# Kernel optimization log

Hardware: AMD Instinct MI355X
Metric: run time of the kernel (lower is better)

The kernel has to match this reference:

```python
import jax, jax.numpy as jnp
import numpy as np

B, L, D, H, VOCAB = 8, 1024, 1024, 8, 32000
DH = D // H  # dim_per_head = 128
SCALE = float((DH // H) ** (-0.5))  # faithful to key.size(-1)//num_heads
EPS = 1e-5


def setup_inputs() -> dict:
    key = jax.random.key(0)
    ks = jax.random.split(key, 12)
    tokens = jax.random.randint(ks[0], (B, L), 0, VOCAB)
    s = 0.02
    emb = jax.random.normal(ks[1], (VOCAB, D), jnp.float32) * s
    emb = emb.at[0].set(0.0)  # padding_idx=0
    Wq = jax.random.normal(ks[2], (D, D), jnp.float32) * s
    Wk = jax.random.normal(ks[3], (D, D), jnp.float32) * s
    Wv = jax.random.normal(ks[4], (D, D), jnp.float32) * s
    Wo = jax.random.normal(ks[5], (D, D), jnp.float32) * s
    bq = jnp.zeros((D,), jnp.float32)
    bk = jnp.zeros((D,), jnp.float32)
    bv = jnp.zeros((D,), jnp.float32)
    bo = jnp.zeros((D,), jnp.float32)
    gamma = jnp.ones((2 * D,), jnp.float32)
    beta = jnp.zeros((2 * D,), jnp.float32)
    return {"tokens": tokens, "emb": emb, "Wq": Wq, "bq": bq, "Wk": Wk,
            "bk": bk, "Wv": Wv, "bv": bv, "Wo": Wo, "bo": bo,
            "gamma": gamma, "beta": beta}


def reference(tokens, emb, Wq, bq, Wk, bk, Wv, bv, Wo, bo, gamma, beta):
    # padding mask: [B, L, L] True where key token == 0
    pad = (tokens == 0)  # [B, L]
    mask = jnp.broadcast_to(pad[:, None, :], (B, L, L))
    mask = jnp.tile(mask, (H, 1, 1))  # torch .repeat(num_heads,1,1) -> [H*B, L, L]

    x = emb[tokens]  # [B, L, D]

    q = (x @ Wq + bq).reshape(B * H, L, DH)  # faithful interleaved view
    k = (x @ Wk + bk).reshape(B * H, L, DH)
    v = (x @ Wv + bv).reshape(B * H, L, DH)

    scores = jnp.einsum('bqd,bkd->bqk', q, k) * SCALE
    scores = jnp.where(mask, -jnp.inf, scores)
    attn = jax.nn.softmax(scores, axis=-1)
    ctx = jnp.einsum('bqk,bkd->bqd', attn, v).reshape(B, L, D)

    out = ctx @ Wo + bo  # [B, L, D]
    r = x + out
    maxpool = r.max(axis=1)   # [B, D]
    meanpool = r.mean(axis=1)  # [B, D]
    agg = jnp.concatenate([maxpool, meanpool], axis=1)  # [B, 2D]

    mu = agg.mean(axis=-1, keepdims=True)
    var = agg.var(axis=-1, keepdims=True)
    return (agg - mu) / jnp.sqrt(var + EPS) * gamma + beta
```

## Files before the change

### kernel.cpp

```cpp
#include <hip/hip_runtime.h>
#include <math.h>

typedef __attribute__((ext_vector_type(8))) short short8;
typedef __attribute__((ext_vector_type(4))) float f32x4;

constexpr int CB = 8, CL = 1024, CD = 1024, CDH = 128, CM = 8192;
constexpr float CSCALE = 0.25f;
constexpr float CEPS = 1e-5f;

__device__ inline ushort f2b(float f) {
    union { float f; unsigned u; } v; v.f = f;
    unsigned r = v.u + 0x7FFF + ((v.u >> 16) & 1);
    return (ushort)(r >> 16);
}
__device__ inline float b2f(ushort u) {
    union { unsigned u; float f; } v; v.u = ((unsigned)u) << 16;
    return v.f;
}

__device__ inline void gld16(const void* g, void* l) {
    __builtin_amdgcn_global_load_lds(
        (const __attribute__((address_space(1))) void*)g,
        (__attribute__((address_space(3))) void*)l, 16, 0, 0);
}

__global__ __launch_bounds__(256) void k_gather(const int* __restrict__ tokens,
                                                const float* __restrict__ emb,
                                                float* __restrict__ x,
                                                ushort* __restrict__ xb) {
    int row = blockIdx.x;
    int tok = tokens[row];
    float4 v = ((const float4*)(emb + (size_t)tok * CD))[threadIdx.x];
    ((float4*)(x + (size_t)row * CD))[threadIdx.x] = v;
    ushort4 o; o.x = f2b(v.x); o.y = f2b(v.y); o.z = f2b(v.z); o.w = f2b(v.w);
    ((ushort4*)(xb + (size_t)row * CD))[threadIdx.x] = o;
}

__global__ __launch_bounds__(256) void k_wtrans(const float* __restrict__ W,
                                                ushort* __restrict__ Wt) {
    __shared__ float ws_[32][33];
    const int tk = blockIdx.x * 32, tn = blockIdx.y * 32;
    const int t = threadIdx.x;
    {
        int r = t >> 3, c4 = (t & 7) * 4;
        *(float4*)&ws_[r][c4] = *(const float4*)&W[(size_t)(tk + r) * CD + tn + c4];
    }
    __syncthreads();
    int n = t >> 3, k4 = (t & 7) * 4;
    ushort4 o;
    o.x = f2b(ws_[k4 + 0][n]); o.y = f2b(ws_[k4 + 1][n]);
    o.z = f2b(ws_[k4 + 2][n]); o.w = f2b(ws_[k4 + 3][n]);
    *(ushort4*)&Wt[(size_t)(tn + n) * CD + tk + k4] = o;
}

__global__ __launch_bounds__(256) void k_gemm_qkv(const ushort* __restrict__ A,
                                                  const ushort* __restrict__ Wt3,
                                                  const float* __restrict__ b0,
                                                  const float* __restrict__ b1,
                                                  const float* __restrict__ b2,
                                                  ushort* __restrict__ C3) {
    __shared__ ushort As[128 * 32];
    __shared__ ushort Bs[128 * 32];
    const int z = blockIdx.z;
    const ushort* Bt  = Wt3 + (size_t)z * CD * CD;
    const float* bias = (z == 0) ? b0 : ((z == 1) ? b1 : b2);
    ushort* Cout      = C3 + (size_t)z * CM * CD;

    const int t = threadIdx.x, w = t >> 6, l = t & 63;
    const int lane15 = l & 15, quad = l >> 4;
    const int bm = blockIdx.y * 128, bn = blockIdx.x * 128;
    const int wm = (w >> 1) * 64, wn = (w & 1) * 64;
    const int arow = l >> 2;
    const int aseg = (l & 3) * 8;
    f32x4 acc[4][4] = {};

    for (int k0 = 0; k0 < CD; k0 += 32) {
        __syncthreads();
        #pragma unroll
        for (int c2 = 0; c2 < 2; ++c2) {
            int c = w * 2 + c2;
            gld16(A  + (size_t)(bm + c * 16 + arow) * CD + k0 + aseg, &As[c * 512 + l * 8]);
            gld16(Bt + (size_t)(bn + c * 16 + arow) * CD + k0 + aseg, &Bs[c * 512 + l * 8]);
        }
        __syncthreads();
        short8 af[4], bf[4];
        #pragma unroll
        for (int im = 0; im < 4; ++im)
            af[im] = *(const short8*)&As[(wm + im * 16 + lane15) * 32 + quad * 8];
        #pragma unroll
        for (int in = 0; in < 4; ++in)
            bf[in] = *(const short8*)&Bs[(wn + in * 16 + lane15) * 32 + quad * 8];
        #pragma unroll
        for (int im = 0; im < 4; ++im)
            #pragma unroll
            for (int in = 0; in < 4; ++in)
                acc[im][in] = __builtin_amdgcn_mfma_f32_16x16x32_bf16(af[im], bf[in], acc[im][in], 0, 0, 0);
    }
    #pragma unroll
    for (int in = 0; in < 4; ++in) {
        int col = bn + wn + in * 16 + lane15;
        float bv = bias[col];
        #pragma unroll
        for (int im = 0; im < 4; ++im) {
            int row0 = bm + wm + im * 16 + quad * 4;
            #pragma unroll
            for (int r = 0; r < 4; ++r)
                Cout[(size_t)(row0 + r) * CD + col] = f2b(acc[im][in][r] + bv);
        }
    }
}

__global__ __launch_bounds__(256) void k_gemm_out(const ushort* __restrict__ A,
                                                  const ushort* __restrict__ Bt,
                                                  const float* __restrict__ bias,
                                                  const float* __restrict__ resid,
                                                  float* __restrict__ pmax,
                                                  float* __restrict__ psum) {
    __shared__ ushort As[128 * 32];
    __shared__ ushort Bs[128 * 32];
    __shared__ float redmx[4][64], redsm[4][64];
    const int t = threadIdx.x, w = t >> 6, l = t & 63;
    const int lane15 = l & 15, quad = l >> 4;
    const int bm = blockIdx.y * 128, bn = blockIdx.x * 128;
    const int wm = (w >> 1) * 64, wn = (w & 1) * 64;
    const int arow = l >> 2;
    const int aseg = (l & 3) * 8;
    f32x4 acc[4][4] = {};

    for (int k0 = 0; k0 < CD; k0 += 32) {
        __syncthreads();
        #pragma unroll
        for (int c2 = 0; c2 < 2; ++c2) {
            int c = w * 2 + c2;
            gld16(A  + (size_t)(bm + c * 16 + arow) * CD + k0 + aseg, &As[c * 512 + l * 8]);
            gld16(Bt + (size_t)(bn + c * 16 + arow) * CD + k0 + aseg, &Bs[c * 512 + l * 8]);
        }
        __syncthreads();
        short8 af[4], bf[4];
        #pragma unroll
        for (int im = 0; im < 4; ++im)
            af[im] = *(const short8*)&As[(wm + im * 16 + lane15) * 32 + quad * 8];
        #pragma unroll
        for (int in = 0; in < 4; ++in)
            bf[in] = *(const short8*)&Bs[(wn + in * 16 + lane15) * 32 + quad * 8];
        #pragma unroll
        for (int im = 0; im < 4; ++im)
            #pragma unroll
            for (int in = 0; in < 4; ++in)
                acc[im][in] = __builtin_amdgcn_mfma_f32_16x16x32_bf16(af[im], bf[in], acc[im][in], 0, 0, 0);
    }
    const int by = blockIdx.y, bb = by >> 3, chunk = by & 7;
    float vmax_[4], vsum_[4];
    #pragma unroll
    for (int in = 0; in < 4; ++in) {
        int col = bn + wn + in * 16 + lane15;
        float bvv = bias[col];
        float mx = -3.4e38f, sm = 0.f;
        #pragma unroll
        for (int im = 0; im < 4; ++im) {
            int row0 = bm + wm + im * 16 + quad * 4;
            #pragma unroll
            for (int r = 0; r < 4; ++r) {
                float rel = acc[im][in][r] + bvv + resid[(size_t)(row0 + r) * CD + col];
                mx = fmaxf(mx, rel);
                sm += rel;
            }
        }
        mx = fmaxf(mx, __shfl_xor(mx, 16));
        mx = fmaxf(mx, __shfl_xor(mx, 32));
        sm += __shfl_xor(sm, 16);
        sm += __shfl_xor(sm, 32);
        vmax_[in] = mx; vsum_[in] = sm;
    }
    if (l < 16) {
        #pragma unroll
        for (int in = 0; in < 4; ++in) {
            redmx[w][in * 16 + lane15] = vmax_[in];
            redsm[w][in * 16 + lane15] = vsum_[in];
        }
    }
    __syncthreads();
    if (t < 128) {
        int wcol = t >> 6, cc = t & 63;
        float m = fmaxf(redmx[wcol][cc], redmx[wcol + 2][cc]);
        float s = redsm[wcol][cc] + redsm[wcol + 2][cc];
        size_t off2 = ((size_t)bb * 8 + chunk) * CD + bn + wcol * 64 + cc;
        pmax[off2] = m;
        psum[off2] = s;
    }
}

__global__ __launch_bounds__(256) void k_vtransp(const ushort* __restrict__ v,
                                                 ushort* __restrict__ Vtp) {
    __shared__ ushort Vs[64 * 136];
    const int i = blockIdx.x >> 4, kt = blockIdx.x & 15;
    const ushort* src = v + (size_t)i * 131072 + (size_t)kt * 64 * 128;
    const int t = threadIdx.x;
    #pragma unroll
    for (int ii = 0; ii < 4; ++ii) {
        int idx = t + 256 * ii;
        int key = idx >> 4, seg = idx & 15;
        *(uint4*)&Vs[key * 136 + seg * 8] = *(const uint4*)&src[key * 128 + seg * 8];
    }
    __syncthreads();
    ushort* dst = Vtp + (size_t)blockIdx.x * 8192;
    #pragma unroll
    for (int it = 0; it < 4; ++it) {
        int L = t + 256 * it;
        int cell = L & 63;
        int quadk = cell >> 4, l15 = cell & 15;
        int p = L >> 6;
        int d = (p >> 1) * 16 + l15;
        int kb = ((p & 1) * 4 + quadk) * 8;
        uint pk[4];
        #pragma unroll
        for (int jj = 0; jj < 4; ++jj) {
            uint lo = Vs[(kb + 2 * jj) * 136 + d];
            uint hi = Vs[(kb + 2 * jj + 1) * 136 + d];
            pk[jj] = lo | (hi << 16);
        }
        *(uint4*)&dst[(size_t)L * 8] = *(uint4*)pk;
    }
}

__global__ __launch_bounds__(512) void k_attn(const ushort* __restrict__ Q,
                                              const ushort* __restrict__ K,
                                              const ushort* __restrict__ Vtp,
                                              const int* __restrict__ tokens,
                                              ushort* __restrict__ ctx) {
    __shared__ ushort Ks[16 * 512];
    __shared__ ushort Vs[16 * 512];
    __shared__ ushort Ps[8 * 1088];
    __shared__ ushort Msk[CL];
    const int i = blockIdx.x, qb = blockIdx.y * 128;
    const int t = threadIdx.x, w = t >> 6, l = t & 63;
    const int lane15 = l & 15, quad = l >> 4;

    {
        const int* tokb = tokens + (i & 7) * CL;
        #pragma unroll
        for (int jj = 0; jj < 2; ++jj) {
            int idx = t + 512 * jj;
            Msk[idx] = (tokb[idx] == 0) ? (ushort)0xFF80 : (ushort)0;
        }
    }
    const int qrow = qb + w * 16 + lane15;
    short8 af[4];
    #pragma unroll
    for (int kc = 0; kc < 4; ++kc)
        af[kc] = *(const short8*)&Q[(size_t)i * 131072 + (size_t)qrow * 128 + kc * 32 + quad * 8];

    f32x4 oacc[8];
    #pragma unroll
    for (int dt = 0; dt < 8; ++dt) oacc[dt] = f32x4{0.f, 0.f, 0.f, 0.f};
    float lsum[4] = {0.f, 0.f, 0.f, 0.f};
    const int wbase = w * 1088;

    for (int kt = 0; kt < 16; ++kt) {
        __syncthreads();
        #pragma unroll
        for (int c = 0; c < 2; ++c) {
            int p = w * 2 + c;
            gld16(K + (size_t)i * 131072 + (size_t)(kt * 64 + (p >> 2) * 16 + lane15) * 128
                    + (p & 3) * 32 + quad * 8,
                  &Ks[p * 512 + l * 8]);
            gld16(Vtp + ((size_t)(i * 16 + kt) * 16 + p) * 512 + l * 8,
                  &Vs[p * 512 + l * 8]);
        }
        __syncthreads();

        f32x4 sc[4];
        #pragma unroll
        for (int j = 0; j < 4; ++j) {
            sc[j] = f32x4{0.f, 0.f, 0.f, 0.f};
            #pragma unroll
            for (int kc = 0; kc < 4; ++kc) {
                short8 bk = *(const short8*)&Ks[(j * 4 + kc) * 512 + l * 8];
                sc[j] = __builtin_amdgcn_mfma_f32_16x16x32_bf16(af[kc], bk, sc[j], 0, 0, 0);
            }
        }
        #pragma unroll
        for (int j = 0; j < 4; ++j) {
            float mj = b2f(Msk[kt * 64 + j * 16 + lane15]);
            #pragma unroll
            for (int r = 0; r < 4; ++r) {
                float p = __expf(fmaf(sc[j][r], CSCALE, mj));
                sc[j][r] = p;
                lsum[r] += p;
            }
        }
        #pragma unroll
        for (int j = 0; j < 4; ++j) {
            int ks2 = j >> 1;
            int qq  = (j & 1) * 2 + (lane15 >> 3);
            int pos = lane15 & 7;
            #pragma unroll
            for (int r = 0; r < 4; ++r) {
                union { float f; unsigned u; } cv; cv.f = sc[j][r];
                Ps[wbase + ks2 * 544 + qq * 136 + (quad * 4 + r) * 8 + pos] =
                    (ushort)(cv.u >> 16);
            }
        }
        short8 ap[2];
        #pragma unroll
        for (int ks2 = 0; ks2 < 2; ++ks2)
            ap[ks2] = *(const short8*)&Ps[wbase + ks2 * 544 + quad * 136 + lane15 * 8];
        #pragma unroll
        for (int dt = 0; dt < 8; ++dt)
            #pragma unroll
            for (int ks2 = 0; ks2 < 2; ++ks2) {
                short8 bv = *(const short8*)&Vs[(dt * 2 + ks2) * 512 + l * 8];
                oacc[dt] = __builtin_amdgcn_mfma_f32_16x16x32_bf16(ap[ks2], bv, oacc[dt], 0, 0, 0);
            }
    }
    float inv[4];
    #pragma unroll
    for (int r = 0; r < 4; ++r) {
        float s = lsum[r];
        #pragma unroll
        for (int off = 1; off < 16; off <<= 1) s += __shfl_xor(s, off);
        inv[r] = 1.f / s;
    }
    #pragma unroll
    for (int dt = 0; dt < 8; ++dt)
        #pragma unroll
        for (int r = 0; r < 4; ++r) {
            int q = qb + w * 16 + quad * 4 + r;
            ctx[(size_t)i * 131072 + (size_t)q * 128 + dt * 16 + lane15] =
                f2b(oacc[dt][r] * inv[r]);
        }
}

__global__ __launch_bounds__(1024) void k_pool2(const float* __restrict__ pmax,
                                                const float* __restrict__ psum,
                                                const float* __restrict__ gamma,
                                                const float* __restrict__ beta,
                                                float* __restrict__ out) {
    __shared__ float rs[16], rq[16];
    __shared__ float s_mu, s_inv;
    const int b = blockIdx.x;
    const int d = threadIdx.x;
    float mx = -3.4e38f, sm = 0.f;
    #pragma unroll
    for (int c = 0; c < 8; ++c) {
        size_t off = ((size_t)b * 8 + c) * CD + d;
        mx = fmaxf(mx, pmax[off]);
        sm += psum[off];
    }
    const float a0 = mx;
    const float a1 = sm * (1.0f / 1024.0f);
    float s = a0 + a1;
    float qd = a0 * a0 + a1 * a1;
    #pragma unroll
    for (int off = 32; off > 0; off >>= 1) {
        s  += __shfl_xor(s, off);
        qd += __shfl_xor(qd, off);
    }
    const int wid = d >> 6;
    if ((d & 63) == 0) { rs[wid] = s; rq[wid] = qd; }
    __syncthreads();
    if (d == 0) {
        float S = 0.f, Qm = 0.f;
        for (int ww = 0; ww < 16; ++ww) { S += rs[ww]; Qm += rq[ww]; }
        float mu  = S * (1.0f / 2048.0f);
        float var = Qm * (1.0f / 2048.0f) - mu * mu;
        s_mu = mu; s_inv = 1.0f / sqrtf(var + CEPS);
    }
    __syncthreads();
    const float mu = s_mu, inv = s_inv;
    out[(size_t)b * 2048 + d]        = (a0 - mu) * inv * gamma[d]        + beta[d];
    out[(size_t)b * 2048 + 1024 + d] = (a1 - mu) * inv * gamma[1024 + d] + beta[1024 + d];
}

extern "C" void kernel_launch(void* const* d_in, const int* in_sizes, int n_in,
                              void* d_out, int out_size, void* d_ws, size_t ws_size,
                              hipStream_t stream) {
    const int*   tokens = (const int*)d_in[0];
    const float* emb    = (const float*)d_in[1];
    const float* Wq     = (const float*)d_in[2];
    const float* bq     = (const float*)d_in[3];
    const float* Wk     = (const float*)d_in[4];
    const float* bk     = (const float*)d_in[5];
    const float* Wv     = (const float*)d_in[6];
    const float* bv     = (const float*)d_in[7];
    const float* Wo     = (const float*)d_in[8];
    const float* bo     = (const float*)d_in[9];
    const float* gamma  = (const float*)d_in[10];
    const float* beta   = (const float*)d_in[11];
    float* out = (float*)d_out;

    char* p = (char*)d_ws;
    float*  x   = (float*)p;   p += (size_t)CM * CD * 4;
    ushort* xb  = (ushort*)p;  p += (size_t)CM * CD * 2;
    ushort* wqt = (ushort*)p;  p += (size_t)CD * CD * 2;
    ushort* wkt = (ushort*)p;  p += (size_t)CD * CD * 2;
    ushort* wvt = (ushort*)p;  p += (size_t)CD * CD * 2;
    ushort* wot = (ushort*)p;  p += (size_t)CD * CD * 2;
    ushort* qb_ = (ushort*)p;  p += (size_t)CM * CD * 2;
    ushort* kb_ = (ushort*)p;  p += (size_t)CM * CD * 2;
    ushort* vb_ = (ushort*)p;  p += (size_t)CM * CD * 2;
    ushort* Vtp = (ushort*)p;  p += (size_t)CM * CD * 2;
    float*  pmax = (float*)p;  p += (size_t)CB * 8 * CD * 4;
    float*  psum = (float*)p;  p += (size_t)CB * 8 * CD * 4;
    ushort* ctx = vb_;

    k_gather<<<CM, 256, 0, stream>>>(tokens, emb, x, xb);

    dim3 wg(32, 32);
    k_wtrans<<<wg, 256, 0, stream>>>(Wq, wqt);
    k_wtrans<<<wg, 256, 0, stream>>>(Wk, wkt);
    k_wtrans<<<wg, 256, 0, stream>>>(Wv, wvt);
    k_wtrans<<<wg, 256, 0, stream>>>(Wo, wot);

    dim3 gq(CD / 128, CM / 128, 3);
    k_gemm_qkv<<<gq, 256, 0, stream>>>(xb, wqt, bq, bk, bv, qb_);

    k_vtransp<<<64 * 16, 256, 0, stream>>>(vb_, Vtp);

    dim3 ag(64, 8);
    k_attn<<<ag, 512, 0, stream>>>(qb_, kb_, Vtp, tokens, ctx);

    dim3 go(CD / 128, CM / 128);
    k_gemm_out<<<go, 256, 0, stream>>>(ctx, wot, bo, x, pmax, psum);

    k_pool2<<<CB, 1024, 0, stream>>>(pmax, psum, gamma, beta, out);
}
```

Measured before the change: 366.2 us.

## Double-buffer K/V tiles in attention and give each wave two query groups

The attention kernel now uses 256 threads per block, and each wave handles 32 query rows as two 16-row groups. Each loaded K and V fragment therefore feeds two MFMAs. K/V tiles are double-buffered in LDS, with the next tile's global-to-LDS load issued before computing on the current one, and only one barrier per iteration. This is meant to hide global load latency and halve LDS fragment reads per MFMA. The cost is more registers (two accumulator sets), double the K/V LDS footprint, and fewer waves per block, which may lower occupancy.

```diff
diff --git a/kernel.cpp b/kernel.cpp
--- a/kernel.cpp
+++ b/kernel.cpp
@@ -223,14 +223,30 @@
     }
 }
 
-__global__ __launch_bounds__(512) void k_attn(const ushort* __restrict__ Q,
+__device__ inline void attn_stage(const ushort* __restrict__ K,
+                                  const ushort* __restrict__ Vtp,
+                                  ushort* KsBuf, ushort* VsBuf,
+                                  int i, int kt, int w, int l,
+                                  int lane15, int quad) {
+    #pragma unroll
+    for (int c = 0; c < 4; ++c) {
+        int p = w * 4 + c;
+        gld16(K + (size_t)i * 131072 + (size_t)(kt * 64 + (p >> 2) * 16 + lane15) * 128
+                + (p & 3) * 32 + quad * 8,
+              KsBuf + p * 512 + (size_t)l * 8);
+        gld16(Vtp + ((size_t)(i * 16 + kt) * 16 + p) * 512 + (size_t)l * 8,
+              VsBuf + p * 512 + (size_t)l * 8);
+    }
+}
+
+__global__ __launch_bounds__(256) void k_attn(const ushort* __restrict__ Q,
                                               const ushort* __restrict__ K,
                                               const ushort* __restrict__ Vtp,
                                               const int* __restrict__ tokens,
                                               ushort* __restrict__ ctx) {
-    __shared__ ushort Ks[16 * 512];
-    __shared__ ushort Vs[16 * 512];
-    __shared__ ushort Ps[8 * 1088];
+    __shared__ ushort Ks[2][16 * 512];
+    __shared__ ushort Vs[2][16 * 512];
+    __shared__ ushort Ps[4 * 1088];
     __shared__ ushort Msk[CL];
     const int i = blockIdx.x, qb = blockIdx.y * 128;
     const int t = threadIdx.x, w = t >> 6, l = t & 63;
@@ -239,96 +255,111 @@
     {
         const int* tokb = tokens + (i & 7) * CL;
         #pragma unroll
-        for (int jj = 0; jj < 2; ++jj) {
-            int idx = t + 512 * jj;
+        for (int jj = 0; jj < 4; ++jj) {
+            int idx = t + 256 * jj;
             Msk[idx] = (tokb[idx] == 0) ? (ushort)0xFF80 : (ushort)0;
         }
     }
-    const int qrow = qb + w * 16 + lane15;
-    short8 af[4];
-    #pragma unroll
-    for (int kc = 0; kc < 4; ++kc)
-        af[kc] = *(const short8*)&Q[(size_t)i * 131072 + (size_t)qrow * 128 + kc * 32 + quad * 8];
-
-    f32x4 oacc[8];
-    #pragma unroll
-    for (int dt = 0; dt < 8; ++dt) oacc[dt] = f32x4{0.f, 0.f, 0.f, 0.f};
-    float lsum[4] = {0.f, 0.f, 0.f, 0.f};
+    short8 af[2][4];
+    #pragma unroll
+    for (int g = 0; g < 2; ++g)
+        #pragma unroll
+        for (int kc = 0; kc < 4; ++kc)
+            af[g][kc] = *(const short8*)&Q[(size_t)i * 131072
+                + (size_t)(qb + w * 32 + g * 16 + lane15) * 128 + kc * 32 + quad * 8];
+
+    f32x4 oacc[2][8];
+    #pragma unroll
+    for (int g = 0; g < 2; ++g)
+        #pragma unroll
+        for (int dt = 0; dt < 8; ++dt) oacc[g][dt] = f32x4{0.f, 0.f, 0.f, 0.f};
+    float lsum[2][4] = {};
     const int wbase = w * 1088;
 
+    attn_stage(K, Vtp, Ks[0], Vs[0], i, 0, w, l, lane15, quad);
+    __syncthreads();
+
     for (int kt = 0; kt < 16; ++kt) {
-        __syncthreads();
-        #pragma unroll
-        for (int c = 0; c < 2; ++c) {
-            int p = w * 2 + c;
-            gld16(K + (size_t)i * 131072 + (size_t)(kt * 64 + (p >> 2) * 16 + lane15) * 128
-                    + (p & 3) * 32 + quad * 8,
-                  &Ks[p * 512 + l * 8]);
-            gld16(Vtp + ((size_t)(i * 16 + kt) * 16 + p) * 512 + l * 8,
-                  &Vs[p * 512 + l * 8]);
-        }
-        __syncthreads();
-
-        f32x4 sc[4];
+        const int cur = kt & 1;
+        if (kt < 15)
+            attn_stage(K, Vtp, Ks[cur ^ 1], Vs[cur ^ 1], i, kt + 1, w, l, lane15, quad);
+
+        f32x4 sc[2][4];
         #pragma unroll
         for (int j = 0; j < 4; ++j) {
-            sc[j] = f32x4{0.f, 0.f, 0.f, 0.f};
-            #pragma unroll
-            for (int kc = 0; kc < 4; ++kc) {
-                short8 bk = *(const short8*)&Ks[(j * 4 + kc) * 512 + l * 8];
-                sc[j] = __builtin_amdgcn_mfma_f32_16x16x32_bf16(af[kc], bk, sc[j], 0, 0, 0);
+            short8 bk[4];
+            #pragma unroll
+            for (int kc = 0; kc < 4; ++kc)
+                bk[kc] = *(const short8*)&Ks[cur][(j * 4 + kc) * 512 + l * 8];
+            #pragma unroll
+            for (int g = 0; g < 2; ++g) {
+                sc[g][j] = f32x4{0.f, 0.f, 0.f, 0.f};
+                #pragma unroll
+                for (int kc = 0; kc < 4; ++kc)
+                    sc[g][j] = __builtin_amdgcn_mfma_f32_16x16x32_bf16(af[g][kc], bk[kc], sc[g][j], 0, 0, 0);
             }
         }
         #pragma unroll
         for (int j = 0; j < 4; ++j) {
             float mj = b2f(Msk[kt * 64 + j * 16 + lane15]);
             #pragma unroll
+            for (int g = 0; g < 2; ++g)
+                #pragma unroll
+                for (int r = 0; r < 4; ++r) {
+                    float pv = __expf(fmaf(sc[g][j][r], CSCALE, mj));
+                    sc[g][j][r] = pv;
+                    lsum[g][r] += pv;
+                }
+        }
+        short8 ap[2][2];
+        #pragma unroll
+        for (int g = 0; g < 2; ++g) {
+            #pragma unroll
+            for (int j = 0; j < 4; ++j) {
+                int ks2 = j >> 1;
+                int qq  = (j & 1) * 2 + (lane15 >> 3);
+                int pos = lane15 & 7;
+                #pragma unroll
+                for (int r = 0; r < 4; ++r) {
+                    union { float f; unsigned u; } cv; cv.f = sc[g][j][r];
+                    Ps[wbase + ks2 * 544 + qq * 136 + (quad * 4 + r) * 8 + pos] =
+                        (ushort)(cv.u >> 16);
+                }
+            }
+            #pragma unroll
+            for (int ks2 = 0; ks2 < 2; ++ks2)
+                ap[g][ks2] = *(const short8*)&Ps[wbase + ks2 * 544 + quad * 136 + lane15 * 8];
+        }
+        #pragma unroll
+        for (int dt = 0; dt < 8; ++dt)
+            #pragma unroll
+            for (int ks2 = 0; ks2 < 2; ++ks2) {
+                short8 bv = *(const short8*)&Vs[cur][(dt * 2 + ks2) * 512 + l * 8];
+                #pragma unroll
+                for (int g = 0; g < 2; ++g)
+                    oacc[g][dt] = __builtin_amdgcn_mfma_f32_16x16x32_bf16(ap[g][ks2], bv, oacc[g][dt], 0, 0, 0);
+            }
+        __syncthreads();
+    }
+    #pragma unroll
+    for (int g = 0; g < 2; ++g) {
+        float inv[4];
+        #pragma unroll
+        for (int r = 0; r < 4; ++r) {
+            float s = lsum[g][r];
+            #pragma unroll
+            for (int off = 1; off < 16; off <<= 1) s += __shfl_xor(s, off);
+            inv[r] = 1.f / s;
+        }
+        #pragma unroll
+        for (int dt = 0; dt < 8; ++dt)
+            #pragma unroll
             for (int r = 0; r < 4; ++r) {
-                float p = __expf(fmaf(sc[j][r], CSCALE, mj));
-                sc[j][r] = p;
-                lsum[r] += p;
+                int q = qb + w * 32 + g * 16 + quad * 4 + r;
+                ctx[(size_t)i * 131072 + (size_t)q * 128 + dt * 16 + lane15] =
+                    f2b(oacc[g][dt][r] * inv[r]);
             }
-        }
-        #pragma unroll
-        for (int j = 0; j < 4; ++j) {
-            int ks2 = j >> 1;
-            int qq  = (j & 1) * 2 + (lane15 >> 3);
-            int pos = lane15 & 7;
-            #pragma unroll
-            for (int r = 0; r < 4; ++r) {
-                union { float f; unsigned u; } cv; cv.f = sc[j][r];
-                Ps[wbase + ks2 * 544 + qq * 136 + (quad * 4 + r) * 8 + pos] =
-                    (ushort)(cv.u >> 16);
-            }
-        }
-        short8 ap[2];
-        #pragma unroll
-        for (int ks2 = 0; ks2 < 2; ++ks2)
-            ap[ks2] = *(const short8*)&Ps[wbase + ks2 * 544 + quad * 136 + lane15 * 8];
-        #pragma unroll
-        for (int dt = 0; dt < 8; ++dt)
-            #pragma unroll
-            for (int ks2 = 0; ks2 < 2; ++ks2) {
-                short8 bv = *(const short8*)&Vs[(dt * 2 + ks2) * 512 + l * 8];
-                oacc[dt] = __builtin_amdgcn_mfma_f32_16x16x32_bf16(ap[ks2], bv, oacc[dt], 0, 0, 0);
-            }
-    }
-    float inv[4];
-    #pragma unroll
-    for (int r = 0; r < 4; ++r) {
-        float s = lsum[r];
-        #pragma unroll
-        for (int off = 1; off < 16; off <<= 1) s += __shfl_xor(s, off);
-        inv[r] = 1.f / s;
-    }
-    #pragma unroll
-    for (int dt = 0; dt < 8; ++dt)
-        #pragma unroll
-        for (int r = 0; r < 4; ++r) {
-            int q = qb + w * 16 + quad * 4 + r;
-            ctx[(size_t)i * 131072 + (size_t)q * 128 + dt * 16 + lane15] =
-                f2b(oacc[dt][r] * inv[r]);
-        }
+    }
 }
 
 __global__ __launch_bounds__(1024) void k_pool2(const float* __restrict__ pmax,
@@ -418,7 +449,7 @@
     k_vtransp<<<64 * 16, 256, 0, stream>>>(vb_, Vtp);
 
     dim3 ag(64, 8);
-    k_attn<<<ag, 512, 0, stream>>>(qb_, kb_, Vtp, tokens, ctx);
+    k_attn<<<ag, 256, 0, stream>>>(qb_, kb_, Vtp, tokens, ctx);
 
     dim3 go(CD / 128, CM / 128);
     k_gemm_out<<<go, 256, 0, stream>>>(ctx, wot, bo, x, pmax, psum);
```

After: 366.8 us. No clear change (+0.2%).
